# Optimization experiments

Hardware: AMD Instinct MI355X
Metric: run time of the kernel (lower is better)

The kernel has to match this reference:

```python
import jax, jax.numpy as jnp
import numpy as np

C = 256
C8 = C // 8


def setup_inputs() -> dict:
    key = jax.random.key(0)
    ks = jax.random.split(key, 9)
    B, H, W = 4, 64, 64
    inp = jax.random.normal(ks[0], (B, C, H, W), dtype=jnp.float32)
    original = jax.random.normal(ks[1], (B, C, H, W), dtype=jnp.float32)
    s = 1.0 / np.sqrt(C)
    wq = jax.random.normal(ks[2], (C8, C), dtype=jnp.float32) * s
    bq = jax.random.normal(ks[3], (C8,), dtype=jnp.float32) * 0.01
    wk = jax.random.normal(ks[4], (C8, C), dtype=jnp.float32) * s
    bk = jax.random.normal(ks[5], (C8,), dtype=jnp.float32) * 0.01
    wv = jax.random.normal(ks[6], (C, C), dtype=jnp.float32) * s
    bv = jax.random.normal(ks[7], (C,), dtype=jnp.float32) * 0.01
    # torch inits gamma to 0; use a nonzero value so the attention branch contributes
    gamma = jnp.asarray([0.5], dtype=jnp.float32)
    return {"input": inp, "original": original, "wq": wq, "bq": bq,
            "wk": wk, "bk": bk, "wv": wv, "bv": bv, "gamma": gamma}


def reference(input, original, wq, bq, wk, bk, wv, bv, gamma):
    B, Cc, H, W = input.shape
    HW = H * W
    x = input.reshape(B, Cc, HW)          # [B, C, HW]
    o = original.reshape(B, Cc, HW)
    # 1x1 convs == per-pixel linear projections
    q = jnp.einsum('oc,bcn->bno', wq, x) + bq          # [B, HW, C8]
    k = jnp.einsum('oc,bcn->bon', wk, x) + bk[:, None]  # [B, C8, HW]
    v = jnp.einsum('oc,bcn->bon', wv, o) + bv[:, None]  # [B, C, HW]
    attn = jax.nn.softmax(jnp.einsum('bic,bcj->bij', q, k), axis=-1)  # [B, HW, HW]
    out = jnp.einsum('bcj,bij->bci', v, attn)           # [B, C, HW]
    out = out.reshape(B, Cc, H, W)
    return gamma[0] * out + input
```

## Files before the change

### kernel.cpp

```cpp
#include <hip/hip_runtime.h>

typedef short s16x8 __attribute__((ext_vector_type(8)));
typedef float f32x4 __attribute__((ext_vector_type(4)));
typedef float f32x16 __attribute__((ext_vector_type(16)));

#define B_ 4
#define C_ 256
#define S_ 4096
#define LOG2E 1.44269504088896f
#define M2 32.0f

#if __has_builtin(__builtin_amdgcn_exp2f)
#define EXP2(x) __builtin_amdgcn_exp2f(x)
#else
#define EXP2(x) __exp2f(x)
#endif

__device__ __forceinline__ unsigned short f2b(float f) {
  union { float f; unsigned u; } v; v.f = f;
  unsigned r = v.u + 0x7fffu + ((v.u >> 16) & 1u);
  return (unsigned short)(r >> 16);
}
__device__ __forceinline__ unsigned short f2b_fast(float f) {
  union { float f; unsigned u; } v; v.f = f;
  return (unsigned short)((v.u + 0x8000u) >> 16);
}
__device__ __forceinline__ s16x8 lds_ld8(const unsigned short* p) {
  union { s16x8 v; uint2 u[2]; } r;
  r.u[0] = *(const uint2*)p;
  r.u[1] = *(const uint2*)(p + 4);
  return r.v;
}

__global__ __launch_bounds__(256)
void proj_kernel(const float* __restrict__ x, const float* __restrict__ orig,
                 const float* __restrict__ wq, const float* __restrict__ bq,
                 const float* __restrict__ wk, const float* __restrict__ bk,
                 const float* __restrict__ wv, const float* __restrict__ bv,
                 unsigned short* __restrict__ Qb, unsigned short* __restrict__ Kb,
                 unsigned short* __restrict__ Vf) {
  __shared__ unsigned short Al[64 * 68];
  __shared__ unsigned short Sl[64 * 68];
  const int ct = blockIdx.x >> 6;
  const int jt = blockIdx.x & 63;
  const int n0 = jt * 64;
  const int b  = blockIdx.y;
  const int t  = threadIdx.x;
  const int L = t & 63, w = t >> 6;
  const int mt = w >> 1, nt = w & 1;
  const int g = L >> 5, l32 = L & 31;
  const float* srcb = ((ct == 0) ? x : orig) + (size_t)b * C_ * S_;
  f32x16 acc = (f32x16)0.0f;

  for (int kc = 0; kc < 4; ++kc) {
    const int k0 = kc * 64;
    __syncthreads();
    #pragma unroll
    for (int rep = 0; rep < 4; ++rep) {
      const int idx = rep * 256 + t;
      const int row = idx >> 4, c4 = (idx & 15) * 4;
      const float* wsrc; int wrow;
      if (ct == 0) {
        if (row < 32) { wsrc = wq; wrow = row; } else { wsrc = wk; wrow = row - 32; }
      } else { wsrc = wv; wrow = (ct - 1) * 64 + row; }
      f32x4 v = *(const f32x4*)(wsrc + (size_t)wrow * 256 + k0 + c4);
      union { unsigned short us[4]; uint2 u2; } pk;
      #pragma unroll
      for (int i = 0; i < 4; ++i) pk.us[i] = f2b(v[i]);
      *(uint2*)&Al[row * 68 + c4] = pk.u2;
    }
    {
      const int c4 = (t >> 4) * 4;
      const int n4 = (t & 15) * 4;
      f32x4 v0 = *(const f32x4*)(srcb + (size_t)(k0 + c4 + 0) * S_ + n0 + n4);
      f32x4 v1 = *(const f32x4*)(srcb + (size_t)(k0 + c4 + 1) * S_ + n0 + n4);
      f32x4 v2 = *(const f32x4*)(srcb + (size_t)(k0 + c4 + 2) * S_ + n0 + n4);
      f32x4 v3 = *(const f32x4*)(srcb + (size_t)(k0 + c4 + 3) * S_ + n0 + n4);
      #pragma unroll
      for (int k = 0; k < 4; ++k) {
        union { unsigned short us[4]; uint2 u2; } pk;
        pk.us[0] = f2b(v0[k]); pk.us[1] = f2b(v1[k]);
        pk.us[2] = f2b(v2[k]); pk.us[3] = f2b(v3[k]);
        *(uint2*)&Sl[(n4 + k) * 68 + c4] = pk.u2;
      }
    }
    __syncthreads();
    #pragma unroll
    for (int ks = 0; ks < 4; ++ks) {
      s16x8 af = lds_ld8(&Al[(mt * 32 + l32) * 68 + ks * 16 + g * 8]);
      s16x8 bf = lds_ld8(&Sl[(nt * 32 + l32) * 68 + ks * 16 + g * 8]);
      acc = __builtin_amdgcn_mfma_f32_32x32x16_bf16(af, bf, acc, 0, 0, 0);
    }
  }
  __syncthreads();
  unsigned short* Rl = Al;
  const int n = nt * 32 + l32;
  if (ct == 0) {
    #pragma unroll
    for (int reg = 0; reg < 16; ++reg) {
      const int rr = (reg & 3) + 8 * (reg >> 2) + 4 * g;
      const float val = (mt == 0) ? (acc[reg] + bq[rr]) * LOG2E : acc[reg] + bk[rr];
      Rl[n * 68 + mt * 32 + rr] = f2b(val);
    }
    __syncthreads();
    const int nn = t >> 2, ch0 = (t & 3) * 16;
    s16x8 a = lds_ld8(Rl + nn * 68 + ch0);
    s16x8 c = lds_ld8(Rl + nn * 68 + ch0 + 8);
    unsigned short* dst = (ch0 < 32)
        ? Qb + ((size_t)b * S_ + n0 + nn) * 32 + ch0
        : Kb + ((size_t)b * S_ + n0 + nn) * 32 + (ch0 - 32);
    *(s16x8*)dst = a;
    *(s16x8*)(dst + 8) = c;
  } else {
    const int cg = ct - 1;
    #pragma unroll
    for (int reg = 0; reg < 16; ++reg) {
      const int rr = (reg & 3) + 8 * (reg >> 2) + 4 * g;
      const int ch = mt * 32 + rr;
      Rl[ch * 68 + n] = f2b(acc[reg] + bv[cg * 64 + ch]);
    }
    __syncthreads();
    unsigned short* grp = Vf + ((size_t)(b * 64 + jt) * 4 + cg) * 4096;
    #pragma unroll
    for (int k = 0; k < 2; ++k) {
      const int G = t * 2 + k;
      const int vv = G >> 8, kb = (G >> 6) & 3, Lf = G & 63;
      const int ch64 = vv * 32 + (Lf & 31);
      const int j64  = kb * 16 + (Lf >> 5) * 8;
      s16x8 v = lds_ld8(Rl + ch64 * 68 + j64);
      *(s16x8*)(grp + G * 8) = v;
    }
  }
}

union FlashU {
  unsigned short P[64 * 68];
  float scr[2][32 * 258];
};

__global__ __launch_bounds__(512, 4)
void flash_kernel(const unsigned short* __restrict__ Qb,
                  const unsigned short* __restrict__ Kb,
                  const unsigned short* __restrict__ Vf,
                  const float* __restrict__ inp,
                  const float* __restrict__ gamma,
                  float* __restrict__ out) {
  __shared__ FlashU sm;
  __shared__ float lpart[2][64];
  __shared__ float invl[64];
  const int l  = blockIdx.x;
  const int b  = (l & 7) >> 1;
  const int i0 = ((l >> 3) * 2 + (l & 1)) * 64;
  const int t  = threadIdx.x;
  const int L = t & 63, w = t >> 6;
  const int q4 = L >> 4, c16 = L & 15;
  const int g  = L >> 5, l32 = L & 31;
  const int rh = w & 3, jh = w >> 2;
  const int cg = w & 3, dup = w >> 2;
  const float gam = gamma[0];
  const unsigned short* Kbase = Kb + (size_t)b * S_ * 32;
  const s16x8 qf = *(const s16x8*)(Qb + ((size_t)b * S_ + i0 + rh * 16 + c16) * 32 + q4 * 8);

  f32x16 acc00 = (f32x16)0.0f, acc01 = (f32x16)0.0f;
  f32x16 acc10 = (f32x16)0.0f, acc11 = (f32x16)0.0f;
  float lp[4] = {0.f, 0.f, 0.f, 0.f};

  s16x8 kc0 = *(const s16x8*)(Kbase + (size_t)(jh * 32 + c16) * 32 + q4 * 8);
  s16x8 kc1 = *(const s16x8*)(Kbase + (size_t)(jh * 32 + 16 + c16) * 32 + q4 * 8);

  for (int j0 = 0; j0 < S_; j0 += 64) {
    const int jt = j0 >> 6;
    const int jn = (j0 + 64 < S_) ? j0 + 64 : j0;
    s16x8 kn0 = *(const s16x8*)(Kbase + (size_t)(jn + jh * 32 + c16) * 32 + q4 * 8);
    s16x8 kn1 = *(const s16x8*)(Kbase + (size_t)(jn + jh * 32 + 16 + c16) * 32 + q4 * 8);
    const unsigned short* vbase = Vf + ((size_t)(b * 64 + jt) * 4 + cg) * 4096;
    s16x8 vf00 = *(const s16x8*)(vbase + (dup * 2 + 0) * 512 + L * 8);
    s16x8 vf01 = *(const s16x8*)(vbase + 2048 + (dup * 2 + 0) * 512 + L * 8);
    s16x8 vf10 = *(const s16x8*)(vbase + (dup * 2 + 1) * 512 + L * 8);
    s16x8 vf11 = *(const s16x8*)(vbase + 2048 + (dup * 2 + 1) * 512 + L * 8);
    f32x4 cinit = (f32x4)(-M2);
    f32x4 s0 = __builtin_amdgcn_mfma_f32_16x16x32_bf16(qf, kc0, cinit, 0, 0, 0);
    f32x4 s1 = __builtin_amdgcn_mfma_f32_16x16x32_bf16(qf, kc1, cinit, 0, 0, 0);
    #pragma unroll
    for (int r = 0; r < 4; ++r) {
      const float p0 = EXP2(s0[r]);
      const float p1 = EXP2(s1[r]);
      lp[r] += p0 + p1;
      const int row = rh * 16 + q4 * 4 + r;
      sm.P[row * 68 + jh * 32 + c16]      = f2b_fast(p0);
      sm.P[row * 68 + jh * 32 + 16 + c16] = f2b_fast(p1);
    }
    __syncthreads();
    {
      const int ko0 = (dup * 2 + 0) * 16 + g * 8;
      const s16x8 pf0 = lds_ld8(sm.P + l32 * 68 + ko0);
      const s16x8 pf1 = lds_ld8(sm.P + (32 + l32) * 68 + ko0);
      acc00 = __builtin_amdgcn_mfma_f32_32x32x16_bf16(pf0, vf00, acc00, 0, 0, 0);
      acc01 = __builtin_amdgcn_mfma_f32_32x32x16_bf16(pf0, vf01, acc01, 0, 0, 0);
      acc10 = __builtin_amdgcn_mfma_f32_32x32x16_bf16(pf1, vf00, acc10, 0, 0, 0);
      acc11 = __builtin_amdgcn_mfma_f32_32x32x16_bf16(pf1, vf01, acc11, 0, 0, 0);
    }
    {
      const int ko1 = (dup * 2 + 1) * 16 + g * 8;
      const s16x8 pf0 = lds_ld8(sm.P + l32 * 68 + ko1);
      const s16x8 pf1 = lds_ld8(sm.P + (32 + l32) * 68 + ko1);
      acc00 = __builtin_amdgcn_mfma_f32_32x32x16_bf16(pf0, vf10, acc00, 0, 0, 0);
      acc01 = __builtin_amdgcn_mfma_f32_32x32x16_bf16(pf0, vf11, acc01, 0, 0, 0);
      acc10 = __builtin_amdgcn_mfma_f32_32x32x16_bf16(pf1, vf10, acc10, 0, 0, 0);
      acc11 = __builtin_amdgcn_mfma_f32_32x32x16_bf16(pf1, vf11, acc11, 0, 0, 0);
    }
    __syncthreads();
    kc0 = kn0; kc1 = kn1;
  }
  #pragma unroll
  for (int r = 0; r < 4; ++r) {
    float v = lp[r];
    #pragma unroll
    for (int d = 1; d < 16; d <<= 1) v += __shfl_xor(v, d, 64);
    lp[r] = v;
  }
  if (c16 == 0) {
    #pragma unroll
    for (int r = 0; r < 4; ++r) lpart[jh][rh * 16 + q4 * 4 + r] = lp[r];
  }
  __syncthreads();
  if (t < 64) invl[t] = gam / (lpart[0][t] + lpart[1][t]);
  #pragma unroll
  for (int h = 0; h < 2; ++h) {
    const f32x16 a0 = h ? acc10 : acc00;
    const f32x16 a1 = h ? acc11 : acc01;
    float* pl = sm.scr[dup];
    #pragma unroll
    for (int reg = 0; reg < 16; ++reg) {
      const int rr = (reg & 3) + 8 * (reg >> 2) + 4 * g;
      pl[rr * 258 + cg * 64 + l32]      = a0[reg];
      pl[rr * 258 + cg * 64 + 32 + l32] = a1[reg];
    }
    __syncthreads();
    const int ch = t >> 1;
    const int il16 = (t & 1) * 16;
    #pragma unroll
    for (int q = 0; q < 4; ++q) {
      const int iloc = il16 + q * 4;
      const size_t gi = ((size_t)b * C_ + ch) * S_ + i0 + h * 32 + iloc;
      const f32x4 iv = *(const f32x4*)(inp + gi);
      f32x4 o;
      #pragma unroll
      for (int k = 0; k < 4; ++k) {
        const int il = iloc + k;
        o[k] = (sm.scr[0][il * 258 + ch] + sm.scr[1][il * 258 + ch]) * invl[h * 32 + il] + iv[k];
      }
      *(f32x4*)(out + gi) = o;
    }
    __syncthreads();
  }
}

extern "C" void kernel_launch(void* const* d_in, const int* in_sizes, int n_in,
                              void* d_out, int out_size, void* d_ws, size_t ws_size,
                              hipStream_t stream) {
  const float* inp   = (const float*)d_in[0];
  const float* orig  = (const float*)d_in[1];
  const float* wq    = (const float*)d_in[2];
  const float* bq    = (const float*)d_in[3];
  const float* wk    = (const float*)d_in[4];
  const float* bk    = (const float*)d_in[5];
  const float* wv    = (const float*)d_in[6];
  const float* bv    = (const float*)d_in[7];
  const float* gamma = (const float*)d_in[8];
  float* out = (float*)d_out;

  unsigned short* Qb = (unsigned short*)d_ws;
  unsigned short* Kb = Qb + (size_t)B_ * S_ * 32;
  unsigned short* Vf = Kb + (size_t)B_ * S_ * 32;

  proj_kernel<<<dim3(320, 4), 256, 0, stream>>>(inp, orig, wq, bq, wk, bk, wv, bv, Qb, Kb, Vf);
  flash_kernel<<<256, 512, 0, stream>>>(Qb, Kb, Vf, inp, gamma, out);
}
```

Before: 164.9 us.

## Pre-pack weights, merge V projection per tile, software-pipeline flash P·V loop

A new prep kernel converts the Q/K/V weights to bf16 in MFMA fragment order, with LOG2E folded into Wq. The scratch for this sits in the tail of the output buffer, which the flash kernel overwrites later. The projection kernel now has one block compute all 256 V channels for a spatial tile, so each `orig` tile is loaded and converted once instead of four times, and weight fragments are read straight from global memory instead of being staged in LDS. The flash kernel double-buffers P in LDS and delays the P·V MFMAs by one iteration, which removes one barrier per key tile and overlaps the exp/store of the next tile with the matmul of the previous one. The costs are an extra kernel launch, more LDS and registers in proj, and a more complex prologue and epilogue in flash.

```diff
diff --git a/kernel.cpp b/kernel.cpp
--- a/kernel.cpp
+++ b/kernel.cpp
@@ -33,73 +33,110 @@
 }
 
 __global__ __launch_bounds__(256)
+void prep_kernel(const float* __restrict__ wq, const float* __restrict__ wk,
+                 const float* __restrict__ wv,
+                 unsigned short* __restrict__ Wvf, unsigned short* __restrict__ Wqkf) {
+  const int G = (blockIdx.x * 256 + threadIdx.x) * 4;
+  union { unsigned short us[4]; uint2 u2; } pk;
+  if (G < 65536) {
+    const int e0 = G & 7, lane = (G >> 3) & 63, ks16 = (G >> 9) & 15;
+    const int mt = (G >> 13) & 1, cg = G >> 14;
+    const int row = cg * 64 + mt * 32 + (lane & 31);
+    const int k   = ks16 * 16 + (lane >> 5) * 8 + e0;
+    f32x4 v = *(const f32x4*)(wv + (size_t)row * 256 + k);
+    #pragma unroll
+    for (int i = 0; i < 4; ++i) pk.us[i] = f2b(v[i]);
+    *(uint2*)(Wvf + G) = pk.u2;
+  } else {
+    const int H = G - 65536;
+    const int e0 = H & 7, lane = (H >> 3) & 63, ks16 = (H >> 9) & 15;
+    const int mt = (H >> 13) & 1;
+    const int row = lane & 31;
+    const int k   = ks16 * 16 + (lane >> 5) * 8 + e0;
+    const float* src = mt ? wk : wq;
+    f32x4 v = *(const f32x4*)(src + (size_t)row * 256 + k);
+    if (mt == 0) v = v * LOG2E;
+    #pragma unroll
+    for (int i = 0; i < 4; ++i) pk.us[i] = f2b(v[i]);
+    *(uint2*)(Wqkf + H) = pk.u2;
+  }
+}
+
+__global__ __launch_bounds__(256, 4)
 void proj_kernel(const float* __restrict__ x, const float* __restrict__ orig,
-                 const float* __restrict__ wq, const float* __restrict__ bq,
-                 const float* __restrict__ wk, const float* __restrict__ bk,
-                 const float* __restrict__ wv, const float* __restrict__ bv,
+                 const float* __restrict__ bq, const float* __restrict__ bk,
+                 const float* __restrict__ bv,
+                 const unsigned short* __restrict__ Wqkf,
+                 const unsigned short* __restrict__ Wvf,
                  unsigned short* __restrict__ Qb, unsigned short* __restrict__ Kb,
                  unsigned short* __restrict__ Vf) {
-  __shared__ unsigned short Al[64 * 68];
-  __shared__ unsigned short Sl[64 * 68];
-  const int ct = blockIdx.x >> 6;
-  const int jt = blockIdx.x & 63;
-  const int n0 = jt * 64;
-  const int b  = blockIdx.y;
-  const int t  = threadIdx.x;
+  __shared__ union {
+    unsigned short Sl[64 * 68];
+    unsigned short Rv[4 * 64 * 68];
+  } um;
+  const int jt   = blockIdx.x >> 1;
+  const int type = blockIdx.x & 1;
+  const int b    = blockIdx.y;
+  const int n0   = jt * 64;
+  const int t    = threadIdx.x;
   const int L = t & 63, w = t >> 6;
+  const int g = L >> 5, l32 = L & 31;
+  const float* srcb = (type == 0 ? x : orig) + (size_t)b * C_ * S_;
+  f32x16 acc0 = (f32x16)0.0f, acc1 = (f32x16)0.0f;
+  f32x16 acc2 = (f32x16)0.0f, acc3 = (f32x16)0.0f;
   const int mt = w >> 1, nt = w & 1;
-  const int g = L >> 5, l32 = L & 31;
-  const float* srcb = ((ct == 0) ? x : orig) + (size_t)b * C_ * S_;
-  f32x16 acc = (f32x16)0.0f;
+  const int cg = w;
 
   for (int kc = 0; kc < 4; ++kc) {
     const int k0 = kc * 64;
     __syncthreads();
-    #pragma unroll
-    for (int rep = 0; rep < 4; ++rep) {
-      const int idx = rep * 256 + t;
-      const int row = idx >> 4, c4 = (idx & 15) * 4;
-      const float* wsrc; int wrow;
-      if (ct == 0) {
-        if (row < 32) { wsrc = wq; wrow = row; } else { wsrc = wk; wrow = row - 32; }
-      } else { wsrc = wv; wrow = (ct - 1) * 64 + row; }
-      f32x4 v = *(const f32x4*)(wsrc + (size_t)wrow * 256 + k0 + c4);
-      union { unsigned short us[4]; uint2 u2; } pk;
-      #pragma unroll
-      for (int i = 0; i < 4; ++i) pk.us[i] = f2b(v[i]);
-      *(uint2*)&Al[row * 68 + c4] = pk.u2;
-    }
     {
-      const int c4 = (t >> 4) * 4;
-      const int n4 = (t & 15) * 4;
-      f32x4 v0 = *(const f32x4*)(srcb + (size_t)(k0 + c4 + 0) * S_ + n0 + n4);
-      f32x4 v1 = *(const f32x4*)(srcb + (size_t)(k0 + c4 + 1) * S_ + n0 + n4);
-      f32x4 v2 = *(const f32x4*)(srcb + (size_t)(k0 + c4 + 2) * S_ + n0 + n4);
-      f32x4 v3 = *(const f32x4*)(srcb + (size_t)(k0 + c4 + 3) * S_ + n0 + n4);
+      const int c4s = (t >> 4) * 4;
+      const int n4  = (t & 15) * 4;
+      f32x4 v0 = *(const f32x4*)(srcb + (size_t)(k0 + c4s + 0) * S_ + n0 + n4);
+      f32x4 v1 = *(const f32x4*)(srcb + (size_t)(k0 + c4s + 1) * S_ + n0 + n4);
+      f32x4 v2 = *(const f32x4*)(srcb + (size_t)(k0 + c4s + 2) * S_ + n0 + n4);
+      f32x4 v3 = *(const f32x4*)(srcb + (size_t)(k0 + c4s + 3) * S_ + n0 + n4);
       #pragma unroll
       for (int k = 0; k < 4; ++k) {
         union { unsigned short us[4]; uint2 u2; } pk;
         pk.us[0] = f2b(v0[k]); pk.us[1] = f2b(v1[k]);
         pk.us[2] = f2b(v2[k]); pk.us[3] = f2b(v3[k]);
-        *(uint2*)&Sl[(n4 + k) * 68 + c4] = pk.u2;
-      }
-    }
-    __syncthreads();
-    #pragma unroll
-    for (int ks = 0; ks < 4; ++ks) {
-      s16x8 af = lds_ld8(&Al[(mt * 32 + l32) * 68 + ks * 16 + g * 8]);
-      s16x8 bf = lds_ld8(&Sl[(nt * 32 + l32) * 68 + ks * 16 + g * 8]);
-      acc = __builtin_amdgcn_mfma_f32_32x32x16_bf16(af, bf, acc, 0, 0, 0);
+        *(uint2*)&um.Sl[(n4 + k) * 68 + c4s] = pk.u2;
+      }
+    }
+    __syncthreads();
+    if (type == 0) {
+      #pragma unroll
+      for (int ks = 0; ks < 4; ++ks) {
+        const int ks16 = kc * 4 + ks;
+        s16x8 af = *(const s16x8*)(Wqkf + ((size_t)(mt * 16 + ks16) * 64 + L) * 8);
+        s16x8 bf = lds_ld8(&um.Sl[(nt * 32 + l32) * 68 + ks * 16 + g * 8]);
+        acc0 = __builtin_amdgcn_mfma_f32_32x32x16_bf16(af, bf, acc0, 0, 0, 0);
+      }
+    } else {
+      #pragma unroll
+      for (int ks = 0; ks < 4; ++ks) {
+        const int ks16 = kc * 4 + ks;
+        s16x8 af0 = *(const s16x8*)(Wvf + ((size_t)((cg * 2 + 0) * 16 + ks16) * 64 + L) * 8);
+        s16x8 af1 = *(const s16x8*)(Wvf + ((size_t)((cg * 2 + 1) * 16 + ks16) * 64 + L) * 8);
+        s16x8 bf0 = lds_ld8(&um.Sl[l32 * 68 + ks * 16 + g * 8]);
+        s16x8 bf1 = lds_ld8(&um.Sl[(32 + l32) * 68 + ks * 16 + g * 8]);
+        acc0 = __builtin_amdgcn_mfma_f32_32x32x16_bf16(af0, bf0, acc0, 0, 0, 0);
+        acc1 = __builtin_amdgcn_mfma_f32_32x32x16_bf16(af0, bf1, acc1, 0, 0, 0);
+        acc2 = __builtin_amdgcn_mfma_f32_32x32x16_bf16(af1, bf0, acc2, 0, 0, 0);
+        acc3 = __builtin_amdgcn_mfma_f32_32x32x16_bf16(af1, bf1, acc3, 0, 0, 0);
+      }
     }
   }
   __syncthreads();
-  unsigned short* Rl = Al;
-  const int n = nt * 32 + l32;
-  if (ct == 0) {
+  if (type == 0) {
+    unsigned short* Rl = um.Sl;
+    const int n = nt * 32 + l32;
     #pragma unroll
     for (int reg = 0; reg < 16; ++reg) {
       const int rr = (reg & 3) + 8 * (reg >> 2) + 4 * g;
-      const float val = (mt == 0) ? (acc[reg] + bq[rr]) * LOG2E : acc[reg] + bk[rr];
+      const float val = (mt == 0) ? acc0[reg] + bq[rr] * LOG2E : acc0[reg] + bk[rr];
       Rl[n * 68 + mt * 32 + rr] = f2b(val);
     }
     __syncthreads();
@@ -112,29 +149,35 @@
     *(s16x8*)dst = a;
     *(s16x8*)(dst + 8) = c;
   } else {
-    const int cg = ct - 1;
-    #pragma unroll
-    for (int reg = 0; reg < 16; ++reg) {
-      const int rr = (reg & 3) + 8 * (reg >> 2) + 4 * g;
-      const int ch = mt * 32 + rr;
-      Rl[ch * 68 + n] = f2b(acc[reg] + bv[cg * 64 + ch]);
-    }
-    __syncthreads();
-    unsigned short* grp = Vf + ((size_t)(b * 64 + jt) * 4 + cg) * 4096;
-    #pragma unroll
-    for (int k = 0; k < 2; ++k) {
-      const int G = t * 2 + k;
-      const int vv = G >> 8, kb = (G >> 6) & 3, Lf = G & 63;
-      const int ch64 = vv * 32 + (Lf & 31);
-      const int j64  = kb * 16 + (Lf >> 5) * 8;
-      s16x8 v = lds_ld8(Rl + ch64 * 68 + j64);
-      *(s16x8*)(grp + G * 8) = v;
+    #pragma unroll
+    for (int mi = 0; mi < 2; ++mi)
+      #pragma unroll
+      for (int ni = 0; ni < 2; ++ni) {
+        const f32x16 a = (mi == 0) ? (ni == 0 ? acc0 : acc1) : (ni == 0 ? acc2 : acc3);
+        #pragma unroll
+        for (int reg = 0; reg < 16; ++reg) {
+          const int rr = (reg & 3) + 8 * (reg >> 2) + 4 * g;
+          const int ch = mi * 32 + rr;
+          um.Rv[(cg * 64 + ch) * 68 + ni * 32 + l32] = f2b(a[reg] + bv[cg * 64 + ch]);
+        }
+      }
+    __syncthreads();
+    unsigned short* Vtile = Vf + (size_t)(b * 64 + jt) * 4 * 4096;
+    #pragma unroll
+    for (int k = 0; k < 8; ++k) {
+      const int cI = k * 256 + t;
+      const int cgc = cI >> 9, r = cI & 511;
+      const int vv = r >> 8, kb = (r >> 6) & 3, Lf = r & 63;
+      const int chl = vv * 32 + (Lf & 31);
+      const int jj  = kb * 16 + (Lf >> 5) * 8;
+      s16x8 v = lds_ld8(&um.Rv[(cgc * 64 + chl) * 68 + jj]);
+      *(s16x8*)(Vtile + (size_t)cI * 8) = v;
     }
   }
 }
 
 union FlashU {
-  unsigned short P[64 * 68];
+  unsigned short P[2][64 * 68];
   float scr[2][32 * 258];
 };
 
@@ -159,58 +202,90 @@
   const int cg = w & 3, dup = w >> 2;
   const float gam = gamma[0];
   const unsigned short* Kbase = Kb + (size_t)b * S_ * 32;
+  const unsigned short* Vbb   = Vf + (size_t)b * 64 * 4 * 4096;
   const s16x8 qf = *(const s16x8*)(Qb + ((size_t)b * S_ + i0 + rh * 16 + c16) * 32 + q4 * 8);
 
   f32x16 acc00 = (f32x16)0.0f, acc01 = (f32x16)0.0f;
   f32x16 acc10 = (f32x16)0.0f, acc11 = (f32x16)0.0f;
   float lp[4] = {0.f, 0.f, 0.f, 0.f};
-
+  s16x8 vf00, vf01, vf10, vf11;
   s16x8 kc0 = *(const s16x8*)(Kbase + (size_t)(jh * 32 + c16) * 32 + q4 * 8);
   s16x8 kc1 = *(const s16x8*)(Kbase + (size_t)(jh * 32 + 16 + c16) * 32 + q4 * 8);
 
-  for (int j0 = 0; j0 < S_; j0 += 64) {
-    const int jt = j0 >> 6;
-    const int jn = (j0 + 64 < S_) ? j0 + 64 : j0;
-    s16x8 kn0 = *(const s16x8*)(Kbase + (size_t)(jn + jh * 32 + c16) * 32 + q4 * 8);
-    s16x8 kn1 = *(const s16x8*)(Kbase + (size_t)(jn + jh * 32 + 16 + c16) * 32 + q4 * 8);
-    const unsigned short* vbase = Vf + ((size_t)(b * 64 + jt) * 4 + cg) * 4096;
-    s16x8 vf00 = *(const s16x8*)(vbase + (dup * 2 + 0) * 512 + L * 8);
-    s16x8 vf01 = *(const s16x8*)(vbase + 2048 + (dup * 2 + 0) * 512 + L * 8);
-    s16x8 vf10 = *(const s16x8*)(vbase + (dup * 2 + 1) * 512 + L * 8);
-    s16x8 vf11 = *(const s16x8*)(vbase + 2048 + (dup * 2 + 1) * 512 + L * 8);
+  for (int n = 0; n < 64; ++n) {
+    if (n > 0) {
+      const unsigned short* vbase = Vbb + (size_t)((n - 1) * 4 + cg) * 4096;
+      vf00 = *(const s16x8*)(vbase + (dup * 2 + 0) * 512 + L * 8);
+      vf01 = *(const s16x8*)(vbase + 2048 + (dup * 2 + 0) * 512 + L * 8);
+      vf10 = *(const s16x8*)(vbase + (dup * 2 + 1) * 512 + L * 8);
+      vf11 = *(const s16x8*)(vbase + 2048 + (dup * 2 + 1) * 512 + L * 8);
+    }
     f32x4 cinit = (f32x4)(-M2);
     f32x4 s0 = __builtin_amdgcn_mfma_f32_16x16x32_bf16(qf, kc0, cinit, 0, 0, 0);
     f32x4 s1 = __builtin_amdgcn_mfma_f32_16x16x32_bf16(qf, kc1, cinit, 0, 0, 0);
+    if (n < 63) {
+      const size_t jn = (size_t)(n + 1) * 64;
+      kc0 = *(const s16x8*)(Kbase + (jn + jh * 32 + c16) * 32 + q4 * 8);
+      kc1 = *(const s16x8*)(Kbase + (jn + jh * 32 + 16 + c16) * 32 + q4 * 8);
+    }
+    unsigned short* Pw = sm.P[n & 1];
     #pragma unroll
     for (int r = 0; r < 4; ++r) {
       const float p0 = EXP2(s0[r]);
       const float p1 = EXP2(s1[r]);
       lp[r] += p0 + p1;
       const int row = rh * 16 + q4 * 4 + r;
-      sm.P[row * 68 + jh * 32 + c16]      = f2b_fast(p0);
-      sm.P[row * 68 + jh * 32 + 16 + c16] = f2b_fast(p1);
-    }
-    __syncthreads();
+      Pw[row * 68 + jh * 32 + c16]      = f2b_fast(p0);
+      Pw[row * 68 + jh * 32 + 16 + c16] = f2b_fast(p1);
+    }
+    if (n > 0) {
+      const unsigned short* Pr = sm.P[(n - 1) & 1];
+      {
+        const int ko = (dup * 2 + 0) * 16 + g * 8;
+        const s16x8 pf0 = lds_ld8(Pr + l32 * 68 + ko);
+        const s16x8 pf1 = lds_ld8(Pr + (32 + l32) * 68 + ko);
+        acc00 = __builtin_amdgcn_mfma_f32_32x32x16_bf16(pf0, vf00, acc00, 0, 0, 0);
+        acc01 = __builtin_amdgcn_mfma_f32_32x32x16_bf16(pf0, vf01, acc01, 0, 0, 0);
+        acc10 = __builtin_amdgcn_mfma_f32_32x32x16_bf16(pf1, vf00, acc10, 0, 0, 0);
+        acc11 = __builtin_amdgcn_mfma_f32_32x32x16_bf16(pf1, vf01, acc11, 0, 0, 0);
+      }
+      {
+        const int ko = (dup * 2 + 1) * 16 + g * 8;
+        const s16x8 pf0 = lds_ld8(Pr + l32 * 68 + ko);
+        const s16x8 pf1 = lds_ld8(Pr + (32 + l32) * 68 + ko);
+        acc00 = __builtin_amdgcn_mfma_f32_32x32x16_bf16(pf0, vf10, acc00, 0, 0, 0);
+        acc01 = __builtin_amdgcn_mfma_f32_32x32x16_bf16(pf0, vf11, acc01, 0, 0, 0);
+        acc10 = __builtin_amdgcn_mfma_f32_32x32x16_bf16(pf1, vf10, acc10, 0, 0, 0);
+        acc11 = __builtin_amdgcn_mfma_f32_32x32x16_bf16(pf1, vf11, acc11, 0, 0, 0);
+      }
+    }
+    __syncthreads();
+  }
+  {
+    const unsigned short* vbase = Vbb + (size_t)(63 * 4 + cg) * 4096;
+    vf00 = *(const s16x8*)(vbase + (dup * 2 + 0) * 512 + L * 8);
+    vf01 = *(const s16x8*)(vbase + 2048 + (dup * 2 + 0) * 512 + L * 8);
+    vf10 = *(const s16x8*)(vbase + (dup * 2 + 1) * 512 + L * 8);
+    vf11 = *(const s16x8*)(vbase + 2048 + (dup * 2 + 1) * 512 + L * 8);
+    const unsigned short* Pr = sm.P[1];
     {
-      const int ko0 = (dup * 2 + 0) * 16 + g * 8;
-      const s16x8 pf0 = lds_ld8(sm.P + l32 * 68 + ko0);
-      const s16x8 pf1 = lds_ld8(sm.P + (32 + l32) * 68 + ko0);
+      const int ko = (dup * 2 + 0) * 16 + g * 8;
+      const s16x8 pf0 = lds_ld8(Pr + l32 * 68 + ko);
+      const s16x8 pf1 = lds_ld8(Pr + (32 + l32) * 68 + ko);
       acc00 = __builtin_amdgcn_mfma_f32_32x32x16_bf16(pf0, vf00, acc00, 0, 0, 0);
       acc01 = __builtin_amdgcn_mfma_f32_32x32x16_bf16(pf0, vf01, acc01, 0, 0, 0);
       acc10 = __builtin_amdgcn_mfma_f32_32x32x16_bf16(pf1, vf00, acc10, 0, 0, 0);
       acc11 = __builtin_amdgcn_mfma_f32_32x32x16_bf16(pf1, vf01, acc11, 0, 0, 0);
     }
     {
-      const int ko1 = (dup * 2 + 1) * 16 + g * 8;
-      const s16x8 pf0 = lds_ld8(sm.P + l32 * 68 + ko1);
-      const s16x8 pf1 = lds_ld8(sm.P + (32 + l32) * 68 + ko1);
+      const int ko = (dup * 2 + 1) * 16 + g * 8;
+      const s16x8 pf0 = lds_ld8(Pr + l32 * 68 + ko);
+      const s16x8 pf1 = lds_ld8(Pr + (32 + l32) * 68 + ko);
       acc00 = __builtin_amdgcn_mfma_f32_32x32x16_bf16(pf0, vf10, acc00, 0, 0, 0);
       acc01 = __builtin_amdgcn_mfma_f32_32x32x16_bf16(pf0, vf11, acc01, 0, 0, 0);
       acc10 = __builtin_amdgcn_mfma_f32_32x32x16_bf16(pf1, vf10, acc10, 0, 0, 0);
       acc11 = __builtin_amdgcn_mfma_f32_32x32x16_bf16(pf1, vf11, acc11, 0, 0, 0);
     }
-    __syncthreads();
-    kc0 = kn0; kc1 = kn1;
   }
   #pragma unroll
   for (int r = 0; r < 4; ++r) {
@@ -273,7 +348,10 @@
   unsigned short* Qb = (unsigned short*)d_ws;
   unsigned short* Kb = Qb + (size_t)B_ * S_ * 32;
   unsigned short* Vf = Kb + (size_t)B_ * S_ * 32;
-
-  proj_kernel<<<dim3(320, 4), 256, 0, stream>>>(inp, orig, wq, bq, wk, bk, wv, bv, Qb, Kb, Vf);
+  unsigned short* Wvf  = (unsigned short*)((char*)d_out + (size_t)out_size * 4 - 262144);
+  unsigned short* Wqkf = Wvf + 65536;
+
+  prep_kernel<<<80, 256, 0, stream>>>(wq, wk, wv, Wvf, Wqkf);
+  proj_kernel<<<dim3(128, 4), 256, 0, stream>>>(inp, orig, bq, bk, bv, Wqkf, Wvf, Qb, Kb, Vf);
   flash_kernel<<<256, 512, 0, stream>>>(Qb, Kb, Vf, inp, gamma, out);
 }
```

Result: slower. 236.3 us (+43.3%).
